# Performance work log

Hardware: AMD Instinct MI355X
Metric: run time of the kernel (lower is better)

Reference implementation:

```python
import jax, jax.numpy as jnp
import numpy as np

N_EXPERTS = 8
TOP_K = 2
C = 2048       # n_embd
H = 1024       # expert_intermediate_size
HS = 2048      # shared_expert_intermediate_size
B, T = 1, 512
SCALE = 0.02


def setup_inputs() -> dict:
    key = jax.random.key(0)
    ks = jax.random.split(key, 10)
    x = jax.random.normal(ks[0], (B, T, C), dtype=jnp.float32)
    gate_w = jax.random.normal(ks[1], (N_EXPERTS, C), dtype=jnp.float32) * SCALE
    w_gate = jax.random.normal(ks[2], (N_EXPERTS, H, C), dtype=jnp.float32) * SCALE
    w_up = jax.random.normal(ks[3], (N_EXPERTS, H, C), dtype=jnp.float32) * SCALE
    w_down = jax.random.normal(ks[4], (N_EXPERTS, C, H), dtype=jnp.float32) * SCALE
    sh_gate = jax.random.normal(ks[5], (HS, C), dtype=jnp.float32) * SCALE
    sh_up = jax.random.normal(ks[6], (HS, C), dtype=jnp.float32) * SCALE
    sh_down = jax.random.normal(ks[7], (C, HS), dtype=jnp.float32) * SCALE
    se_gate_w = jax.random.normal(ks[8], (1, C), dtype=jnp.float32) * SCALE
    return {"x": x, "gate_w": gate_w, "w_gate": w_gate, "w_up": w_up,
            "w_down": w_down, "sh_gate": sh_gate, "sh_up": sh_up,
            "sh_down": sh_down, "se_gate_w": se_gate_w}


def reference(x, gate_w, w_gate, w_up, w_down, sh_gate, sh_up, sh_down, se_gate_w):
    Bb, Tt, Cc = x.shape
    xf = x.reshape(-1, Cc)                      # (t, d)
    # routing
    scores = xf @ gate_w.T                      # (t, E)
    ew, ei = jax.lax.top_k(scores, TOP_K)       # (t, A)
    ew = jax.nn.softmax(ew, axis=-1)
    # expert FFN (dense over experts; identical math to per-token gathered einsum)
    x1 = jax.nn.silu(jnp.einsum('td,ehd->teh', xf, w_gate))
    x3 = jnp.einsum('td,ehd->teh', xf, w_up)
    expert_out = jnp.einsum('teh,edh->ted', x1 * x3, w_down)  # (t, E, d)
    # combine: routed[t] = sum_a ew[t,a] * expert_out[t, ei[t,a]]
    onehot = jax.nn.one_hot(ei, N_EXPERTS, dtype=ew.dtype)    # (t, A, E)
    comb = jnp.einsum('ta,tae->te', ew, onehot)               # (t, E)
    routed = jnp.einsum('te,ted->td', comb, expert_out)
    # shared expert (SwiGLU MLP)
    shared = (jax.nn.silu(xf @ sh_gate.T) * (xf @ sh_up.T)) @ sh_down.T
    sgate = jax.nn.sigmoid(xf @ se_gate_w.T)                  # (t, 1)
    return (routed + sgate * shared).reshape(Bb, Tt, Cc)
```

## Files before the change

kernel.cpp:

```cpp
#include <hip/hip_runtime.h>

typedef unsigned short u16;
typedef u16 u16x8 __attribute__((ext_vector_type(8)));
typedef __bf16 bf16x8 __attribute__((ext_vector_type(8)));
typedef float f32x4 __attribute__((ext_vector_type(4)));

#define NE 8

__device__ __forceinline__ unsigned pk2(float a, float b) {
  unsigned ua = __builtin_bit_cast(unsigned, a) + 0x8000u;
  unsigned ub = __builtin_bit_cast(unsigned, b) + 0x8000u;
  return __builtin_amdgcn_perm(ub, ua, 0x07060302);
}
__device__ __forceinline__ u16 f2bf(float f) {
  return (u16)((__builtin_bit_cast(unsigned, f) + 0x8000u) >> 16);
}
__device__ __forceinline__ bf16x8 ldfrag(const u16* p) {
  union { u16x8 u; bf16x8 b; } x;
  x.u = *(const u16x8*)p;
  return x.b;
}
__device__ __forceinline__ void gld16(const void* g, void* l) {
  __builtin_amdgcn_global_load_lds(
      (const __attribute__((address_space(1))) unsigned int*)g,
      (__attribute__((address_space(3))) unsigned int*)l, 16, 0, 0);
}
#define MFMA16 __builtin_amdgcn_mfma_f32_16x16x32_bf16

__global__ __launch_bounds__(64) void route_prep_kernel(
    const float* __restrict__ x, const float* __restrict__ gw,
    const float* __restrict__ segw, int* __restrict__ counts,
    int* __restrict__ ptok, float* __restrict__ pw, float* __restrict__ sgate,
    u16* __restrict__ xb) {
  int t = blockIdx.x;
  int lane = threadIdx.x;
  const float* xr = x + (size_t)t * 2048;
  u16* xbr = xb + (size_t)t * 2048;
  float s[NE];
#pragma unroll
  for (int e = 0; e < NE; e++) s[e] = 0.f;
  float sg = 0.f;
#pragma unroll
  for (int it = 0; it < 8; it++) {
    int c = it * 256 + lane * 4;
    f32x4 xv = *(const f32x4*)(xr + c);
    *(uint2*)(xbr + c) = make_uint2(pk2(xv[0], xv[1]), pk2(xv[2], xv[3]));
#pragma unroll
    for (int e = 0; e < NE; e++) {
      f32x4 wv4 = *(const f32x4*)(gw + e * 2048 + c);
      s[e] += xv[0] * wv4[0] + xv[1] * wv4[1] + xv[2] * wv4[2] + xv[3] * wv4[3];
    }
    f32x4 sv = *(const f32x4*)(segw + c);
    sg += xv[0] * sv[0] + xv[1] * sv[1] + xv[2] * sv[2] + xv[3] * sv[3];
  }
#pragma unroll
  for (int off = 32; off > 0; off >>= 1) {
#pragma unroll
    for (int e = 0; e < NE; e++) s[e] += __shfl_down(s[e], off);
    sg += __shfl_down(sg, off);
  }
  if (lane == 0) {
    int i0 = 0;
#pragma unroll
    for (int e = 1; e < NE; e++) if (s[e] > s[i0]) i0 = e;
    int i1 = (i0 == 0) ? 1 : 0;
#pragma unroll
    for (int e = 0; e < NE; e++) if (e != i0 && s[e] > s[i1]) i1 = e;
    float r = __expf(s[i1] - s[i0]);
    float w0 = 1.f / (1.f + r);
    float w1 = 1.f - w0;
    int s0 = atomicAdd(&counts[i0], 1);
    ptok[(i0 << 9) + s0] = t; pw[(i0 << 9) + s0] = w0;
    int s1 = atomicAdd(&counts[i1], 1);
    ptok[(i1 << 9) + s1] = t; pw[(i1 << 9) + s1] = w1;
    sgate[t] = 1.f / (1.f + __expf(-sg));
  }
}

__global__ __launch_bounds__(256) void gateup_kernel(
    const u16* __restrict__ xb, const float* __restrict__ Wg,
    const float* __restrict__ Wu, const float* __restrict__ SWg,
    const float* __restrict__ SWu, u16* __restrict__ hbufB,
    u16* __restrict__ hsB, const int* __restrict__ ptok,
    const int* __restrict__ counts) {
  __shared__ __align__(16) u16 As[2][128 * 64];
  __shared__ __align__(16) u16 Bs[2][32 * 64];

  int b = blockIdx.x;
  int t = threadIdx.x;
  int is_ex = (b < 2048);
  int e = 0, j, mt, cnt;
  const float *gW, *uW;
  u16* obase;
  if (is_ex) {
    e = b & 7; j = (b >> 3) & 63; mt = b >> 9;
    cnt = counts[e];
    if (mt * 128 >= cnt) return;
    gW = Wg + (size_t)(e * 1024 + j * 16) * 2048;
    uW = Wu + (size_t)(e * 1024 + j * 16) * 2048;
    obase = hbufB + (size_t)(e * 64 + j) * 8192;
  } else {
    int bs = b - 2048;
    int xcd = bs & 7; mt = (bs >> 3) & 3; j = (bs >> 5) * 8 + xcd; cnt = 512;
    gW = SWg + (size_t)(j * 16) * 2048;
    uW = SWu + (size_t)(j * 16) * 2048;
    obase = hsB + (size_t)j * 8192;
  }

  int lane = t & 63, wv = t >> 6;
  int quad = lane >> 4, l16 = lane & 15;

  const u16* aptr[4];
  int aoff[4];
#pragma unroll
  for (int i = 0; i < 4; i++) {
    int c = 4 * wv + i;
    int row = 8 * c + (lane >> 3);
    int slot = mt * 128 + row;
    int tok = is_ex ? ((slot < cnt) ? ptok[(e << 9) + slot] : 0) : slot;
    aptr[i] = xb + (size_t)tok * 2048 + (((lane & 7) ^ ((lane >> 3) & 7)) * 8);
    aoff[i] = c * 512;
  }
  const float* bsrc[2];
  int bwr[2];
#pragma unroll
  for (int i = 0; i < 2; i++) {
    int rloc = wv * 8 + i * 4 + quad;
    const float* base = (rloc < 16) ? (gW + (size_t)rloc * 2048)
                                    : (uW + (size_t)(rloc - 16) * 2048);
    bsrc[i] = base + l16 * 4;
    bwr[i] = rloc * 64 + (((l16 >> 1) ^ (rloc & 7)) * 8) + ((l16 & 1) * 4);
  }

  f32x4 accg[2] = {}, accu[2] = {};

#define GU_ISSUE(kt1, nb)                                                   \
  f32x4 bv0 = *(const f32x4*)(bsrc[0] + (kt1) * 64);                        \
  f32x4 bv1 = *(const f32x4*)(bsrc[1] + (kt1) * 64);                        \
  _Pragma("unroll") for (int i = 0; i < 4; i++)                             \
      gld16(aptr[i] + (kt1) * 64, &As[nb][aoff[i]]);                        \
  __builtin_amdgcn_sched_barrier(0);

#define GU_FINISH(nb)                                                       \
  asm volatile("s_waitcnt vmcnt(4)" ::: "memory");                          \
  *(uint2*)(&Bs[nb][bwr[0]]) =                                              \
      make_uint2(pk2(bv0[0], bv0[1]), pk2(bv0[2], bv0[3]));                 \
  *(uint2*)(&Bs[nb][bwr[1]]) =                                              \
      make_uint2(pk2(bv1[0], bv1[1]), pk2(bv1[2], bv1[3]));                 \
  asm volatile("s_waitcnt vmcnt(0) lgkmcnt(0)" ::: "memory");               \
  __builtin_amdgcn_s_barrier();                                             \
  __builtin_amdgcn_sched_barrier(0);

#define GU_COMPUTE(pb)                                                      \
  _Pragma("unroll") for (int k2 = 0; k2 < 2; k2++) {                        \
    int sl = ((k2 * 4 + quad) ^ (l16 & 7)) * 8;                             \
    bf16x8 af0 = ldfrag(&As[pb][(wv * 32 + l16) * 64 + sl]);                \
    bf16x8 af1 = ldfrag(&As[pb][(wv * 32 + 16 + l16) * 64 + sl]);           \
    bf16x8 bg = ldfrag(&Bs[pb][l16 * 64 + sl]);                             \
    bf16x8 bu = ldfrag(&Bs[pb][(16 + l16) * 64 + sl]);                      \
    accg[0] = MFMA16(af0, bg, accg[0], 0, 0, 0);                            \
    accg[1] = MFMA16(af1, bg, accg[1], 0, 0, 0);                            \
    accu[0] = MFMA16(af0, bu, accu[0], 0, 0, 0);                            \
    accu[1] = MFMA16(af1, bu, accu[1], 0, 0, 0);                            \
  }

  { GU_ISSUE(0, 0); GU_FINISH(0); }
  int pb = 0;
  for (int kt = 0; kt < 31; kt++) {
    GU_ISSUE(kt + 1, pb ^ 1);
    GU_COMPUTE(pb);
    GU_FINISH(pb ^ 1);
    pb ^= 1;
  }
  GU_COMPUTE(pb);
#undef GU_ISSUE
#undef GU_FINISH
#undef GU_COMPUTE

#pragma unroll
  for (int i = 0; i < 2; i++)
#pragma unroll
    for (int g = 0; g < 4; g++) {
      int rloc = wv * 32 + i * 16 + quad * 4 + g;
      int slot = mt * 128 + rloc;
      if (slot < cnt) {
        float gv = accg[i][g], uv = accu[i][g];
        float h = gv / (1.f + __expf(-gv)) * uv;
        obase[(size_t)slot * 16 + l16] = f2bf(h);
      }
    }
}

__global__ __launch_bounds__(256) void down_kernel(
    const u16* __restrict__ hbufB, const u16* __restrict__ hsB,
    const float* __restrict__ Wd, const float* __restrict__ SWd,
    float* __restrict__ out, const int* __restrict__ ptok,
    const float* __restrict__ pw, const int* __restrict__ counts,
    const float* __restrict__ sgate) {
  __shared__ __align__(16) u16 As[2][4 * 128 * 16];
  __shared__ __align__(16) u16 Bs[2][32 * 64];

  int b = blockIdx.x;
  int t = threadIdx.x;
  int lane = t & 63, wv = t >> 6;
  int quad = lane >> 4, l16 = lane & 15;

  if (b < 2048) {
    int e = b & 7, nt = (b >> 3) & 63, mt = b >> 9;
    int cnt = counts[e];
    if (mt * 128 >= cnt) return;
    const u16* hb = hbufB + (size_t)e * 524288;

    const u16* aptr[4];
    int aoff[4];
#pragma unroll
    for (int i = 0; i < 4; i++) {
      aptr[i] = hb + (size_t)wv * 8192 +
                (size_t)(mt * 128 + i * 32 + (lane >> 1)) * 16 +
                (((lane & 1) ^ ((lane >> 3) & 1)) * 8);
      aoff[i] = wv * 2048 + i * 512;
    }
    const float* bsrc[2];
    int bwr[2];
#pragma unroll
    for (int i = 0; i < 2; i++) {
      int rloc = wv * 8 + i * 4 + quad;
      bsrc[i] = Wd + (size_t)(e * 2048 + nt * 32 + rloc) * 1024 + l16 * 4;
      bwr[i] = rloc * 64 + (((l16 >> 1) ^ (rloc & 7)) * 8) + ((l16 & 1) * 4);
    }

    f32x4 acc[2][2] = {};

#define DE_ISSUE(kt1, nb)                                                   \
  f32x4 bv0 = *(const f32x4*)(bsrc[0] + (kt1) * 64);                        \
  f32x4 bv1 = *(const f32x4*)(bsrc[1] + (kt1) * 64);                        \
  _Pragma("unroll") for (int i = 0; i < 4; i++)                             \
      gld16(aptr[i] + (size_t)(kt1) * 32768, &As[nb][aoff[i]]);             \
  __builtin_amdgcn_sched_barrier(0);

#define DE_FINISH(nb)                                                       \
  asm volatile("s_waitcnt vmcnt(4)" ::: "memory");                          \
  *(uint2*)(&Bs[nb][bwr[0]]) =                                              \
      make_uint2(pk2(bv0[0], bv0[1]), pk2(bv0[2], bv0[3]));                 \
  *(uint2*)(&Bs[nb][bwr[1]]) =                                              \
      make_uint2(pk2(bv1[0], bv1[1]), pk2(bv1[2], bv1[3]));                 \
  asm volatile("s_waitcnt vmcnt(0) lgkmcnt(0)" ::: "memory");               \
  __builtin_amdgcn_s_barrier();                                             \
  __builtin_amdgcn_sched_barrier(0);

#define DE_COMPUTE(pb)                                                      \
  _Pragma("unroll") for (int k2 = 0; k2 < 2; k2++) {                        \
    int jsec = (k2 * 2 + (quad >> 1)) * 2048 +                              \
               (((quad & 1) ^ ((l16 >> 2) & 1)) * 8);                       \
    int sl = ((k2 * 4 + quad) ^ (l16 & 7)) * 8;                             \
    bf16x8 af0 = ldfrag(&As[pb][jsec + (wv * 32 + l16) * 16]);              \
    bf16x8 af1 = ldfrag(&As[pb][jsec + (wv * 32 + 16 + l16) * 16]);         \
    bf16x8 b0 = ldfrag(&Bs[pb][l16 * 64 + sl]);                             \
    bf16x8 b1 = ldfrag(&Bs[pb][(16 + l16) * 64 + sl]);                      \
    acc[0][0] = MFMA16(af0, b0, acc[0][0], 0, 0, 0);                        \
    acc[0][1] = MFMA16(af0, b1, acc[0][1], 0, 0, 0);                        \
    acc[1][0] = MFMA16(af1, b0, acc[1][0], 0, 0, 0);                        \
    acc[1][1] = MFMA16(af1, b1, acc[1][1], 0, 0, 0);                        \
  }

    { DE_ISSUE(0, 0); DE_FINISH(0); }
    int pb = 0;
    for (int kt = 0; kt < 15; kt++) {
      DE_ISSUE(kt + 1, pb ^ 1);
      DE_COMPUTE(pb);
      DE_FINISH(pb ^ 1);
      pb ^= 1;
    }
    DE_COMPUTE(pb);
#undef DE_ISSUE
#undef DE_FINISH
#undef DE_COMPUTE

#pragma unroll
    for (int i = 0; i < 2; i++)
#pragma unroll
      for (int jf = 0; jf < 2; jf++)
#pragma unroll
        for (int g = 0; g < 4; g++) {
          int sl = mt * 128 + wv * 32 + i * 16 + quad * 4 + g;
          if (sl < cnt) {
            int tok = ptok[(e << 9) + sl];
            int col = nt * 32 + jf * 16 + l16;
            atomicAdd(&out[(size_t)tok * 2048 + col],
                      pw[(e << 9) + sl] * acc[i][jf][g]);
          }
        }
  } else {
    int bs = b - 2048;
    int xcd = bs & 7, mt = (bs >> 3) & 3, nt = (bs >> 5) * 8 + xcd;

    const u16* aptr[4];
    int aoff[4];
#pragma unroll
    for (int i = 0; i < 4; i++) {
      aptr[i] = hsB + (size_t)wv * 8192 +
                (size_t)(mt * 128 + i * 32 + (lane >> 1)) * 16 +
                (((lane & 1) ^ ((lane >> 3) & 1)) * 8);
      aoff[i] = wv * 2048 + i * 512;
    }
    int rloc = wv * 4 + quad;
    const float* bsrc = SWd + (size_t)(nt * 16 + rloc) * 2048 + l16 * 4;
    int bwr = rloc * 64 + (((l16 >> 1) ^ (rloc & 7)) * 8) + ((l16 & 1) * 4);

    f32x4 acc[2] = {};

#define DS_ISSUE(kt1, nb)                                                   \
  f32x4 bv0 = *(const f32x4*)(bsrc + (kt1) * 64);                           \
  _Pragma("unroll") for (int i = 0; i < 4; i++)                             \
      gld16(aptr[i] + (size_t)(kt1) * 32768, &As[nb][aoff[i]]);             \
  __builtin_amdgcn_sched_barrier(0);

#define DS_FINISH(nb)                                                       \
  asm volatile("s_waitcnt vmcnt(4)" ::: "memory");                          \
  *(uint2*)(&Bs[nb][bwr]) =                                                 \
      make_uint2(pk2(bv0[0], bv0[1]), pk2(bv0[2], bv0[3]));                 \
  asm volatile("s_waitcnt vmcnt(0) lgkmcnt(0)" ::: "memory");               \
  __builtin_amdgcn_s_barrier();                                             \
  __builtin_amdgcn_sched_barrier(0);

#define DS_COMPUTE(pb)                                                      \
  _Pragma("unroll") for (int k2 = 0; k2 < 2; k2++) {                        \
    int jsec = (k2 * 2 + (quad >> 1)) * 2048 +                              \
               (((quad & 1) ^ ((l16 >> 2) & 1)) * 8);                       \
    int sl = ((k2 * 4 + quad) ^ (l16 & 7)) * 8;                             \
    bf16x8 af0 = ldfrag(&As[pb][jsec + (wv * 32 + l16) * 16]);              \
    bf16x8 af1 = ldfrag(&As[pb][jsec + (wv * 32 + 16 + l16) * 16]);         \
    bf16x8 bb = ldfrag(&Bs[pb][l16 * 64 + sl]);                             \
    acc[0] = MFMA16(af0, bb, acc[0], 0, 0, 0);                              \
    acc[1] = MFMA16(af1, bb, acc[1], 0, 0, 0);                              \
  }

    { DS_ISSUE(0, 0); DS_FINISH(0); }
    int pb = 0;
    for (int kt = 0; kt < 31; kt++) {
      DS_ISSUE(kt + 1, pb ^ 1);
      DS_COMPUTE(pb);
      DS_FINISH(pb ^ 1);
      pb ^= 1;
    }
    DS_COMPUTE(pb);
#undef DS_ISSUE
#undef DS_FINISH
#undef DS_COMPUTE

#pragma unroll
    for (int i = 0; i < 2; i++)
#pragma unroll
      for (int g = 0; g < 4; g++) {
        int row = mt * 128 + wv * 32 + i * 16 + quad * 4 + g;
        atomicAdd(&out[(size_t)row * 2048 + nt * 16 + l16],
                  sgate[row] * acc[i][g]);
      }
  }
}

extern "C" void kernel_launch(void* const* d_in, const int* in_sizes, int n_in,
                              void* d_out, int out_size, void* d_ws, size_t ws_size,
                              hipStream_t stream) {
  const float* x = (const float*)d_in[0];
  const float* gate_w = (const float*)d_in[1];
  const float* w_gate = (const float*)d_in[2];
  const float* w_up = (const float*)d_in[3];
  const float* w_down = (const float*)d_in[4];
  const float* sh_gate = (const float*)d_in[5];
  const float* sh_up = (const float*)d_in[6];
  const float* sh_down = (const float*)d_in[7];
  const float* se_gate_w = (const float*)d_in[8];
  float* out = (float*)d_out;

  char* ws = (char*)d_ws;
  int* counts = (int*)(ws + 0);
  int* ptok = (int*)(ws + 1024);
  float* pw = (float*)(ws + 1024 + 16384);
  float* sg = (float*)(ws + 1024 + 32768);
  u16* xb = (u16*)(ws + 65536);
  u16* hbufB = (u16*)(ws + 65536 + (2u << 20));
  u16* hsB = (u16*)(ws + 65536 + (10u << 20));

  hipMemsetAsync(counts, 0, 32, stream);
  hipMemsetAsync(out, 0, out_size, stream);
  route_prep_kernel<<<512, 64, 0, stream>>>(x, gate_w, se_gate_w, counts,
                                            ptok, pw, sg, xb);
  gateup_kernel<<<2560, 256, 0, stream>>>(xb, w_gate, w_up, sh_gate, sh_up,
                                          hbufB, hsB, ptok, counts);
  down_kernel<<<2560, 256, 0, stream>>>(hbufB, hsB, w_down, sh_down, out,
                                        ptok, pw, counts, sg);
}
```

Before: 347.8 us.

## Widen N tile to 64 and add triple-buffered LDS pipeline in MoE GEMMs

Both the gate/up and down kernels now compute 64-column weight tiles per block instead of 32, so each loaded activation tile is reused across twice as many columns and the grid shrinks accordingly. The double-buffered loop is replaced by a three-stage LDS ring with prefetch two k-steps ahead and a relaxed vmcnt wait, which lets weight loads overlap more compute. This raises register pressure (8 accumulators plus two staging register sets) and LDS use. It also gives fewer blocks, which may hurt occupancy and load balance across CUs.

```diff
diff --git a/kernel.cpp b/kernel.cpp
--- a/kernel.cpp
+++ b/kernel.cpp
@@ -83,28 +83,28 @@
     const float* __restrict__ SWu, u16* __restrict__ hbufB,
     u16* __restrict__ hsB, const int* __restrict__ ptok,
     const int* __restrict__ counts) {
-  __shared__ __align__(16) u16 As[2][128 * 64];
-  __shared__ __align__(16) u16 Bs[2][32 * 64];
+  __shared__ __align__(16) u16 As[3 * 8192];
+  __shared__ __align__(16) u16 Bs[3 * 4096];
 
   int b = blockIdx.x;
   int t = threadIdx.x;
-  int is_ex = (b < 2048);
+  int is_ex = (b < 1024);
   int e = 0, j, mt, cnt;
   const float *gW, *uW;
   u16* obase;
   if (is_ex) {
-    e = b & 7; j = (b >> 3) & 63; mt = b >> 9;
+    e = b & 7; j = (b >> 3) & 31; mt = b >> 8;
     cnt = counts[e];
     if (mt * 128 >= cnt) return;
-    gW = Wg + (size_t)(e * 1024 + j * 16) * 2048;
-    uW = Wu + (size_t)(e * 1024 + j * 16) * 2048;
-    obase = hbufB + (size_t)(e * 64 + j) * 8192;
+    gW = Wg + (size_t)(e * 1024 + j * 32) * 2048;
+    uW = Wu + (size_t)(e * 1024 + j * 32) * 2048;
+    obase = hbufB + (size_t)(e * 64 + 2 * j) * 8192;
   } else {
-    int bs = b - 2048;
+    int bs = b - 1024;
     int xcd = bs & 7; mt = (bs >> 3) & 3; j = (bs >> 5) * 8 + xcd; cnt = 512;
-    gW = SWg + (size_t)(j * 16) * 2048;
-    uW = SWu + (size_t)(j * 16) * 2048;
-    obase = hsB + (size_t)j * 8192;
+    gW = SWg + (size_t)(j * 32) * 2048;
+    uW = SWu + (size_t)(j * 32) * 2048;
+    obase = hsB + (size_t)(2 * j) * 8192;
   }
 
   int lane = t & 63, wv = t >> 6;
@@ -121,74 +121,114 @@
     aptr[i] = xb + (size_t)tok * 2048 + (((lane & 7) ^ ((lane >> 3) & 7)) * 8);
     aoff[i] = c * 512;
   }
-  const float* bsrc[2];
-  int bwr[2];
-#pragma unroll
-  for (int i = 0; i < 2; i++) {
-    int rloc = wv * 8 + i * 4 + quad;
-    const float* base = (rloc < 16) ? (gW + (size_t)rloc * 2048)
-                                    : (uW + (size_t)(rloc - 16) * 2048);
+  const float* bsrc[4];
+  int bwr[4];
+#pragma unroll
+  for (int i = 0; i < 4; i++) {
+    int rloc = wv * 16 + i * 4 + quad;
+    const float* base = (rloc < 32) ? (gW + (size_t)rloc * 2048)
+                                    : (uW + (size_t)(rloc - 32) * 2048);
     bsrc[i] = base + l16 * 4;
     bwr[i] = rloc * 64 + (((l16 >> 1) ^ (rloc & 7)) * 8) + ((l16 & 1) * 4);
   }
 
-  f32x4 accg[2] = {}, accu[2] = {};
-
-#define GU_ISSUE(kt1, nb)                                                   \
-  f32x4 bv0 = *(const f32x4*)(bsrc[0] + (kt1) * 64);                        \
-  f32x4 bv1 = *(const f32x4*)(bsrc[1] + (kt1) * 64);                        \
-  _Pragma("unroll") for (int i = 0; i < 4; i++)                             \
-      gld16(aptr[i] + (kt1) * 64, &As[nb][aoff[i]]);                        \
-  __builtin_amdgcn_sched_barrier(0);
-
-#define GU_FINISH(nb)                                                       \
-  asm volatile("s_waitcnt vmcnt(4)" ::: "memory");                          \
-  *(uint2*)(&Bs[nb][bwr[0]]) =                                              \
-      make_uint2(pk2(bv0[0], bv0[1]), pk2(bv0[2], bv0[3]));                 \
-  *(uint2*)(&Bs[nb][bwr[1]]) =                                              \
-      make_uint2(pk2(bv1[0], bv1[1]), pk2(bv1[2], bv1[3]));                 \
-  asm volatile("s_waitcnt vmcnt(0) lgkmcnt(0)" ::: "memory");               \
-  __builtin_amdgcn_s_barrier();                                             \
-  __builtin_amdgcn_sched_barrier(0);
-
-#define GU_COMPUTE(pb)                                                      \
+  f32x4 bA0, bA1, bA2, bA3, bB0, bB1, bB2, bB3;
+  f32x4 acc00 = {}, acc01 = {}, acc02 = {}, acc03 = {};
+  f32x4 acc10 = {}, acc11 = {}, acc12 = {}, acc13 = {};
+
+#define GU_ISSUE(kt1, ao, S)                                                \
+  S##0 = *(const f32x4*)(bsrc[0] + (kt1) * 64);                             \
+  S##1 = *(const f32x4*)(bsrc[1] + (kt1) * 64);                             \
+  S##2 = *(const f32x4*)(bsrc[2] + (kt1) * 64);                             \
+  S##3 = *(const f32x4*)(bsrc[3] + (kt1) * 64);                             \
+  gld16(aptr[0] + (kt1) * 64, &As[(ao) + aoff[0]]);                         \
+  gld16(aptr[1] + (kt1) * 64, &As[(ao) + aoff[1]]);                         \
+  gld16(aptr[2] + (kt1) * 64, &As[(ao) + aoff[2]]);                         \
+  gld16(aptr[3] + (kt1) * 64, &As[(ao) + aoff[3]]);                         \
+  __builtin_amdgcn_sched_barrier(0);
+
+#define GU_WRITEB(ao, S)                                                    \
+  *(uint2*)(&Bs[((ao) >> 1) + bwr[0]]) =                                    \
+      make_uint2(pk2(S##0[0], S##0[1]), pk2(S##0[2], S##0[3]));             \
+  *(uint2*)(&Bs[((ao) >> 1) + bwr[1]]) =                                    \
+      make_uint2(pk2(S##1[0], S##1[1]), pk2(S##1[2], S##1[3]));             \
+  *(uint2*)(&Bs[((ao) >> 1) + bwr[2]]) =                                    \
+      make_uint2(pk2(S##2[0], S##2[1]), pk2(S##2[2], S##2[3]));             \
+  *(uint2*)(&Bs[((ao) >> 1) + bwr[3]]) =                                    \
+      make_uint2(pk2(S##3[0], S##3[1]), pk2(S##3[2], S##3[3]));
+
+#define GU_COMPUTE(ao)                                                      \
   _Pragma("unroll") for (int k2 = 0; k2 < 2; k2++) {                        \
     int sl = ((k2 * 4 + quad) ^ (l16 & 7)) * 8;                             \
-    bf16x8 af0 = ldfrag(&As[pb][(wv * 32 + l16) * 64 + sl]);                \
-    bf16x8 af1 = ldfrag(&As[pb][(wv * 32 + 16 + l16) * 64 + sl]);           \
-    bf16x8 bg = ldfrag(&Bs[pb][l16 * 64 + sl]);                             \
-    bf16x8 bu = ldfrag(&Bs[pb][(16 + l16) * 64 + sl]);                      \
-    accg[0] = MFMA16(af0, bg, accg[0], 0, 0, 0);                            \
-    accg[1] = MFMA16(af1, bg, accg[1], 0, 0, 0);                            \
-    accu[0] = MFMA16(af0, bu, accu[0], 0, 0, 0);                            \
-    accu[1] = MFMA16(af1, bu, accu[1], 0, 0, 0);                            \
-  }
-
-  { GU_ISSUE(0, 0); GU_FINISH(0); }
-  int pb = 0;
-  for (int kt = 0; kt < 31; kt++) {
-    GU_ISSUE(kt + 1, pb ^ 1);
-    GU_COMPUTE(pb);
-    GU_FINISH(pb ^ 1);
-    pb ^= 1;
-  }
-  GU_COMPUTE(pb);
+    bf16x8 af0 = ldfrag(&As[(ao) + (wv * 32 + l16) * 64 + sl]);             \
+    bf16x8 af1 = ldfrag(&As[(ao) + (wv * 32 + 16 + l16) * 64 + sl]);        \
+    bf16x8 bf0 = ldfrag(&Bs[((ao) >> 1) + l16 * 64 + sl]);                  \
+    bf16x8 bf1 = ldfrag(&Bs[((ao) >> 1) + (16 + l16) * 64 + sl]);           \
+    bf16x8 bf2 = ldfrag(&Bs[((ao) >> 1) + (32 + l16) * 64 + sl]);           \
+    bf16x8 bf3 = ldfrag(&Bs[((ao) >> 1) + (48 + l16) * 64 + sl]);           \
+    acc00 = MFMA16(af0, bf0, acc00, 0, 0, 0);                               \
+    acc01 = MFMA16(af0, bf1, acc01, 0, 0, 0);                               \
+    acc02 = MFMA16(af0, bf2, acc02, 0, 0, 0);                               \
+    acc03 = MFMA16(af0, bf3, acc03, 0, 0, 0);                               \
+    acc10 = MFMA16(af1, bf0, acc10, 0, 0, 0);                               \
+    acc11 = MFMA16(af1, bf1, acc11, 0, 0, 0);                               \
+    acc12 = MFMA16(af1, bf2, acc12, 0, 0, 0);                               \
+    acc13 = MFMA16(af1, bf3, acc13, 0, 0, 0);                               \
+  }
+
+#define GU_PHASE(kt, aoC, aoI, aoW, Si, Sw)                                 \
+  GU_ISSUE((kt) + 2, aoI, Si)                                               \
+  GU_COMPUTE(aoC)                                                           \
+  asm volatile("s_waitcnt vmcnt(8)" ::: "memory");                          \
+  __builtin_amdgcn_sched_barrier(0);                                        \
+  GU_WRITEB(aoW, Sw)                                                        \
+  asm volatile("s_waitcnt lgkmcnt(0)" ::: "memory");                        \
+  __builtin_amdgcn_s_barrier();                                             \
+  __builtin_amdgcn_sched_barrier(0);
+
+  int o0 = 0, o1 = 8192, o2 = 16384;
+  GU_ISSUE(0, o0, bA)
+  GU_ISSUE(1, o1, bB)
+  asm volatile("s_waitcnt vmcnt(8)" ::: "memory");
+  __builtin_amdgcn_sched_barrier(0);
+  GU_WRITEB(o0, bA)
+  asm volatile("s_waitcnt lgkmcnt(0)" ::: "memory");
+  __builtin_amdgcn_s_barrier();
+  __builtin_amdgcn_sched_barrier(0);
+
+  for (int kt = 0; kt < 30; kt += 2) {
+    GU_PHASE(kt, o0, o2, o1, bA, bB)
+    GU_PHASE(kt + 1, o1, o0, o2, bB, bA)
+    int tmp = o0; o0 = o2; o2 = o1; o1 = tmp;
+  }
+  GU_COMPUTE(o0)
+  asm volatile("s_waitcnt vmcnt(0)" ::: "memory");
+  __builtin_amdgcn_sched_barrier(0);
+  GU_WRITEB(o1, bB)
+  asm volatile("s_waitcnt lgkmcnt(0)" ::: "memory");
+  __builtin_amdgcn_s_barrier();
+  __builtin_amdgcn_sched_barrier(0);
+  GU_COMPUTE(o1)
 #undef GU_ISSUE
-#undef GU_FINISH
+#undef GU_WRITEB
 #undef GU_COMPUTE
-
-#pragma unroll
-  for (int i = 0; i < 2; i++)
-#pragma unroll
-    for (int g = 0; g < 4; g++) {
-      int rloc = wv * 32 + i * 16 + quad * 4 + g;
-      int slot = mt * 128 + rloc;
-      if (slot < cnt) {
-        float gv = accg[i][g], uv = accu[i][g];
-        float h = gv / (1.f + __expf(-gv)) * uv;
-        obase[(size_t)slot * 16 + l16] = f2bf(h);
-      }
-    }
+#undef GU_PHASE
+
+#define GU_EPI(AG, AU, i, n)                                                \
+  _Pragma("unroll") for (int g = 0; g < 4; g++) {                           \
+    int rloc = wv * 32 + (i) * 16 + quad * 4 + g;                           \
+    int slot = mt * 128 + rloc;                                             \
+    if (slot < cnt) {                                                       \
+      float gv = AG[g], uv = AU[g];                                         \
+      float h = gv / (1.f + __expf(-gv)) * uv;                              \
+      obase[(size_t)(n) * 8192 + slot * 16 + l16] = f2bf(h);                \
+    }                                                                       \
+  }
+  GU_EPI(acc00, acc02, 0, 0)
+  GU_EPI(acc01, acc03, 0, 1)
+  GU_EPI(acc10, acc12, 1, 0)
+  GU_EPI(acc11, acc13, 1, 1)
+#undef GU_EPI
 }
 
 __global__ __launch_bounds__(256) void down_kernel(
@@ -197,16 +237,88 @@
     float* __restrict__ out, const int* __restrict__ ptok,
     const float* __restrict__ pw, const int* __restrict__ counts,
     const float* __restrict__ sgate) {
-  __shared__ __align__(16) u16 As[2][4 * 128 * 16];
-  __shared__ __align__(16) u16 Bs[2][32 * 64];
+  __shared__ __align__(16) u16 As[3 * 8192];
+  __shared__ __align__(16) u16 Bs[3 * 4096];
 
   int b = blockIdx.x;
   int t = threadIdx.x;
   int lane = t & 63, wv = t >> 6;
   int quad = lane >> 4, l16 = lane & 15;
 
-  if (b < 2048) {
-    int e = b & 7, nt = (b >> 3) & 63, mt = b >> 9;
+#define DN_ISSUE(kt1, ao, S)                                                \
+  S##0 = *(const f32x4*)(bsrc[0] + (kt1) * 64);                             \
+  S##1 = *(const f32x4*)(bsrc[1] + (kt1) * 64);                             \
+  S##2 = *(const f32x4*)(bsrc[2] + (kt1) * 64);                             \
+  S##3 = *(const f32x4*)(bsrc[3] + (kt1) * 64);                             \
+  gld16(aptr[0] + (size_t)(kt1) * 32768, &As[(ao) + aoff[0]]);              \
+  gld16(aptr[1] + (size_t)(kt1) * 32768, &As[(ao) + aoff[1]]);              \
+  gld16(aptr[2] + (size_t)(kt1) * 32768, &As[(ao) + aoff[2]]);              \
+  gld16(aptr[3] + (size_t)(kt1) * 32768, &As[(ao) + aoff[3]]);              \
+  __builtin_amdgcn_sched_barrier(0);
+
+#define DN_WRITEB(ao, S)                                                    \
+  *(uint2*)(&Bs[((ao) >> 1) + bwr[0]]) =                                    \
+      make_uint2(pk2(S##0[0], S##0[1]), pk2(S##0[2], S##0[3]));             \
+  *(uint2*)(&Bs[((ao) >> 1) + bwr[1]]) =                                    \
+      make_uint2(pk2(S##1[0], S##1[1]), pk2(S##1[2], S##1[3]));             \
+  *(uint2*)(&Bs[((ao) >> 1) + bwr[2]]) =                                    \
+      make_uint2(pk2(S##2[0], S##2[1]), pk2(S##2[2], S##2[3]));             \
+  *(uint2*)(&Bs[((ao) >> 1) + bwr[3]]) =                                    \
+      make_uint2(pk2(S##3[0], S##3[1]), pk2(S##3[2], S##3[3]));
+
+#define DN_COMPUTE(ao)                                                      \
+  _Pragma("unroll") for (int k2 = 0; k2 < 2; k2++) {                        \
+    int jsec = (k2 * 2 + (quad >> 1)) * 2048 +                              \
+               (((quad & 1) ^ ((l16 >> 2) & 1)) * 8);                       \
+    int sl = ((k2 * 4 + quad) ^ (l16 & 7)) * 8;                             \
+    bf16x8 af0 = ldfrag(&As[(ao) + jsec + (wv * 32 + l16) * 16]);           \
+    bf16x8 af1 = ldfrag(&As[(ao) + jsec + (wv * 32 + 16 + l16) * 16]);      \
+    bf16x8 bf0 = ldfrag(&Bs[((ao) >> 1) + l16 * 64 + sl]);                  \
+    bf16x8 bf1 = ldfrag(&Bs[((ao) >> 1) + (16 + l16) * 64 + sl]);           \
+    bf16x8 bf2 = ldfrag(&Bs[((ao) >> 1) + (32 + l16) * 64 + sl]);           \
+    bf16x8 bf3 = ldfrag(&Bs[((ao) >> 1) + (48 + l16) * 64 + sl]);           \
+    acc00 = MFMA16(af0, bf0, acc00, 0, 0, 0);                               \
+    acc01 = MFMA16(af0, bf1, acc01, 0, 0, 0);                               \
+    acc02 = MFMA16(af0, bf2, acc02, 0, 0, 0);                               \
+    acc03 = MFMA16(af0, bf3, acc03, 0, 0, 0);                               \
+    acc10 = MFMA16(af1, bf0, acc10, 0, 0, 0);                               \
+    acc11 = MFMA16(af1, bf1, acc11, 0, 0, 0);                               \
+    acc12 = MFMA16(af1, bf2, acc12, 0, 0, 0);                               \
+    acc13 = MFMA16(af1, bf3, acc13, 0, 0, 0);                               \
+  }
+
+#define DN_PHASE(kt, aoC, aoI, aoW, Si, Sw)                                 \
+  DN_ISSUE((kt) + 2, aoI, Si)                                               \
+  DN_COMPUTE(aoC)                                                           \
+  asm volatile("s_waitcnt vmcnt(8)" ::: "memory");                          \
+  __builtin_amdgcn_sched_barrier(0);                                        \
+  DN_WRITEB(aoW, Sw)                                                        \
+  asm volatile("s_waitcnt lgkmcnt(0)" ::: "memory");                        \
+  __builtin_amdgcn_s_barrier();                                             \
+  __builtin_amdgcn_sched_barrier(0);
+
+#define DN_PROLOGUE                                                         \
+  DN_ISSUE(0, o0, bA)                                                       \
+  DN_ISSUE(1, o1, bB)                                                       \
+  asm volatile("s_waitcnt vmcnt(8)" ::: "memory");                          \
+  __builtin_amdgcn_sched_barrier(0);                                        \
+  DN_WRITEB(o0, bA)                                                         \
+  asm volatile("s_waitcnt lgkmcnt(0)" ::: "memory");                        \
+  __builtin_amdgcn_s_barrier();                                             \
+  __builtin_amdgcn_sched_barrier(0);
+
+#define DN_TAIL                                                             \
+  DN_COMPUTE(o0)                                                            \
+  asm volatile("s_waitcnt vmcnt(0)" ::: "memory");                          \
+  __builtin_amdgcn_sched_barrier(0);                                        \
+  DN_WRITEB(o1, bB)                                                         \
+  asm volatile("s_waitcnt lgkmcnt(0)" ::: "memory");                        \
+  __builtin_amdgcn_s_barrier();                                             \
+  __builtin_amdgcn_sched_barrier(0);                                        \
+  DN_COMPUTE(o1)
+
+  if (b < 1024) {
+    int e = b & 7, nt = (b >> 3) & 31, mt = b >> 8;
     int cnt = counts[e];
     if (mt * 128 >= cnt) return;
     const u16* hb = hbufB + (size_t)e * 524288;
@@ -220,78 +332,42 @@
                 (((lane & 1) ^ ((lane >> 3) & 1)) * 8);
       aoff[i] = wv * 2048 + i * 512;
     }
-    const float* bsrc[2];
-    int bwr[2];
-#pragma unroll
-    for (int i = 0; i < 2; i++) {
-      int rloc = wv * 8 + i * 4 + quad;
-      bsrc[i] = Wd + (size_t)(e * 2048 + nt * 32 + rloc) * 1024 + l16 * 4;
+    const float* bsrc[4];
+    int bwr[4];
+#pragma unroll
+    for (int i = 0; i < 4; i++) {
+      int rloc = wv * 16 + i * 4 + quad;
+      bsrc[i] = Wd + (size_t)(e * 2048 + nt * 64 + rloc) * 1024 + l16 * 4;
       bwr[i] = rloc * 64 + (((l16 >> 1) ^ (rloc & 7)) * 8) + ((l16 & 1) * 4);
     }
 
-    f32x4 acc[2][2] = {};
-
-#define DE_ISSUE(kt1, nb)                                                   \
-  f32x4 bv0 = *(const f32x4*)(bsrc[0] + (kt1) * 64);                        \
-  f32x4 bv1 = *(const f32x4*)(bsrc[1] + (kt1) * 64);                        \
-  _Pragma("unroll") for (int i = 0; i < 4; i++)                             \
-      gld16(aptr[i] + (size_t)(kt1) * 32768, &As[nb][aoff[i]]);             \
-  __builtin_amdgcn_sched_barrier(0);
-
-#define DE_FINISH(nb)                                                       \
-  asm volatile("s_waitcnt vmcnt(4)" ::: "memory");                          \
-  *(uint2*)(&Bs[nb][bwr[0]]) =                                              \
-      make_uint2(pk2(bv0[0], bv0[1]), pk2(bv0[2], bv0[3]));                 \
-  *(uint2*)(&Bs[nb][bwr[1]]) =                                              \
-      make_uint2(pk2(bv1[0], bv1[1]), pk2(bv1[2], bv1[3]));                 \
-  asm volatile("s_waitcnt vmcnt(0) lgkmcnt(0)" ::: "memory");               \
-  __builtin_amdgcn_s_barrier();                                             \
-  __builtin_amdgcn_sched_barrier(0);
-
-#define DE_COMPUTE(pb)                                                      \
-  _Pragma("unroll") for (int k2 = 0; k2 < 2; k2++) {                        \
-    int jsec = (k2 * 2 + (quad >> 1)) * 2048 +                              \
-               (((quad & 1) ^ ((l16 >> 2) & 1)) * 8);                       \
-    int sl = ((k2 * 4 + quad) ^ (l16 & 7)) * 8;                             \
-    bf16x8 af0 = ldfrag(&As[pb][jsec + (wv * 32 + l16) * 16]);              \
-    bf16x8 af1 = ldfrag(&As[pb][jsec + (wv * 32 + 16 + l16) * 16]);         \
-    bf16x8 b0 = ldfrag(&Bs[pb][l16 * 64 + sl]);                             \
-    bf16x8 b1 = ldfrag(&Bs[pb][(16 + l16) * 64 + sl]);                      \
-    acc[0][0] = MFMA16(af0, b0, acc[0][0], 0, 0, 0);                        \
-    acc[0][1] = MFMA16(af0, b1, acc[0][1], 0, 0, 0);                        \
-    acc[1][0] = MFMA16(af1, b0, acc[1][0], 0, 0, 0);                        \
-    acc[1][1] = MFMA16(af1, b1, acc[1][1], 0, 0, 0);                        \
-  }
-
-    { DE_ISSUE(0, 0); DE_FINISH(0); }
-    int pb = 0;
-    for (int kt = 0; kt < 15; kt++) {
-      DE_ISSUE(kt + 1, pb ^ 1);
-      DE_COMPUTE(pb);
-      DE_FINISH(pb ^ 1);
-      pb ^= 1;
-    }
-    DE_COMPUTE(pb);
-#undef DE_ISSUE
-#undef DE_FINISH
-#undef DE_COMPUTE
-
-#pragma unroll
-    for (int i = 0; i < 2; i++)
-#pragma unroll
-      for (int jf = 0; jf < 2; jf++)
-#pragma unroll
-        for (int g = 0; g < 4; g++) {
-          int sl = mt * 128 + wv * 32 + i * 16 + quad * 4 + g;
-          if (sl < cnt) {
-            int tok = ptok[(e << 9) + sl];
-            int col = nt * 32 + jf * 16 + l16;
-            atomicAdd(&out[(size_t)tok * 2048 + col],
-                      pw[(e << 9) + sl] * acc[i][jf][g]);
-          }
-        }
+    f32x4 bA0, bA1, bA2, bA3, bB0, bB1, bB2, bB3;
+    f32x4 acc00 = {}, acc01 = {}, acc02 = {}, acc03 = {};
+    f32x4 acc10 = {}, acc11 = {}, acc12 = {}, acc13 = {};
+
+    int o0 = 0, o1 = 8192, o2 = 16384;
+    DN_PROLOGUE
+    for (int kt = 0; kt < 14; kt += 2) {
+      DN_PHASE(kt, o0, o2, o1, bA, bB)
+      DN_PHASE(kt + 1, o1, o0, o2, bB, bA)
+      int tmp = o0; o0 = o2; o2 = o1; o1 = tmp;
+    }
+    DN_TAIL
+
+#define DE_EPI(ACC, i, n)                                                   \
+  _Pragma("unroll") for (int g = 0; g < 4; g++) {                           \
+    int sl = mt * 128 + wv * 32 + (i) * 16 + quad * 4 + g;                  \
+    if (sl < cnt) {                                                         \
+      atomicAdd(&out[(size_t)ptok[(e << 9) + sl] * 2048 + nt * 64 +         \
+                     (n) * 16 + l16],                                       \
+                pw[(e << 9) + sl] * ACC[g]);                                \
+    }                                                                       \
+  }
+    DE_EPI(acc00, 0, 0) DE_EPI(acc01, 0, 1) DE_EPI(acc02, 0, 2) DE_EPI(acc03, 0, 3)
+    DE_EPI(acc10, 1, 0) DE_EPI(acc11, 1, 1) DE_EPI(acc12, 1, 2) DE_EPI(acc13, 1, 3)
+#undef DE_EPI
   } else {
-    int bs = b - 2048;
+    int bs = b - 1024;
     int xcd = bs & 7, mt = (bs >> 3) & 3, nt = (bs >> 5) * 8 + xcd;
 
     const u16* aptr[4];
@@ -303,60 +379,44 @@
                 (((lane & 1) ^ ((lane >> 3) & 1)) * 8);
       aoff[i] = wv * 2048 + i * 512;
     }
-    int rloc = wv * 4 + quad;
-    const float* bsrc = SWd + (size_t)(nt * 16 + rloc) * 2048 + l16 * 4;
-    int bwr = rloc * 64 + (((l16 >> 1) ^ (rloc & 7)) * 8) + ((l16 & 1) * 4);
-
-    f32x4 acc[2] = {};
-
-#define DS_ISSUE(kt1, nb)                                                   \
-  f32x4 bv0 = *(const f32x4*)(bsrc + (kt1) * 64);                           \
-  _Pragma("unroll") for (int i = 0; i < 4; i++)                             \
-      gld16(aptr[i] + (size_t)(kt1) * 32768, &As[nb][aoff[i]]);             \
-  __builtin_amdgcn_sched_barrier(0);
-
-#define DS_FINISH(nb)                                                       \
-  asm volatile("s_waitcnt vmcnt(4)" ::: "memory");                          \
-  *(uint2*)(&Bs[nb][bwr]) =                                                 \
-      make_uint2(pk2(bv0[0], bv0[1]), pk2(bv0[2], bv0[3]));                 \
-  asm volatile("s_waitcnt vmcnt(0) lgkmcnt(0)" ::: "memory");               \
-  __builtin_amdgcn_s_barrier();                                             \
-  __builtin_amdgcn_sched_barrier(0);
-
-#define DS_COMPUTE(pb)                                                      \
-  _Pragma("unroll") for (int k2 = 0; k2 < 2; k2++) {                        \
-    int jsec = (k2 * 2 + (quad >> 1)) * 2048 +                              \
-               (((quad & 1) ^ ((l16 >> 2) & 1)) * 8);                       \
-    int sl = ((k2 * 4 + quad) ^ (l16 & 7)) * 8;                             \
-    bf16x8 af0 = ldfrag(&As[pb][jsec + (wv * 32 + l16) * 16]);              \
-    bf16x8 af1 = ldfrag(&As[pb][jsec + (wv * 32 + 16 + l16) * 16]);         \
-    bf16x8 bb = ldfrag(&Bs[pb][l16 * 64 + sl]);                             \
-    acc[0] = MFMA16(af0, bb, acc[0], 0, 0, 0);                              \
-    acc[1] = MFMA16(af1, bb, acc[1], 0, 0, 0);                              \
-  }
-
-    { DS_ISSUE(0, 0); DS_FINISH(0); }
-    int pb = 0;
-    for (int kt = 0; kt < 31; kt++) {
-      DS_ISSUE(kt + 1, pb ^ 1);
-      DS_COMPUTE(pb);
-      DS_FINISH(pb ^ 1);
-      pb ^= 1;
-    }
-    DS_COMPUTE(pb);
-#undef DS_ISSUE
-#undef DS_FINISH
-#undef DS_COMPUTE
-
-#pragma unroll
-    for (int i = 0; i < 2; i++)
-#pragma unroll
-      for (int g = 0; g < 4; g++) {
-        int row = mt * 128 + wv * 32 + i * 16 + quad * 4 + g;
-        atomicAdd(&out[(size_t)row * 2048 + nt * 16 + l16],
-                  sgate[row] * acc[i][g]);
-      }
-  }
+    const float* bsrc[4];
+    int bwr[4];
+#pragma unroll
+    for (int i = 0; i < 4; i++) {
+      int rloc = wv * 16 + i * 4 + quad;
+      bsrc[i] = SWd + (size_t)(nt * 64 + rloc) * 2048 + l16 * 4;
+      bwr[i] = rloc * 64 + (((l16 >> 1) ^ (rloc & 7)) * 8) + ((l16 & 1) * 4);
+    }
+
+    f32x4 bA0, bA1, bA2, bA3, bB0, bB1, bB2, bB3;
+    f32x4 acc00 = {}, acc01 = {}, acc02 = {}, acc03 = {};
+    f32x4 acc10 = {}, acc11 = {}, acc12 = {}, acc13 = {};
+
+    int o0 = 0, o1 = 8192, o2 = 16384;
+    DN_PROLOGUE
+    for (int kt = 0; kt < 30; kt += 2) {
+      DN_PHASE(kt, o0, o2, o1, bA, bB)
+      DN_PHASE(kt + 1, o1, o0, o2, bB, bA)
+      int tmp = o0; o0 = o2; o2 = o1; o1 = tmp;
+    }
+    DN_TAIL
+
+#define DS_EPI(ACC, i, n)                                                   \
+  _Pragma("unroll") for (int g = 0; g < 4; g++) {                           \
+    int row = mt * 128 + wv * 32 + (i) * 16 + quad * 4 + g;                 \
+    atomicAdd(&out[(size_t)row * 2048 + nt * 64 + (n) * 16 + l16],          \
+              sgate[row] * ACC[g]);                                         \
+  }
+    DS_EPI(acc00, 0, 0) DS_EPI(acc01, 0, 1) DS_EPI(acc02, 0, 2) DS_EPI(acc03, 0, 3)
+    DS_EPI(acc10, 1, 0) DS_EPI(acc11, 1, 1) DS_EPI(acc12, 1, 2) DS_EPI(acc13, 1, 3)
+#undef DS_EPI
+  }
+#undef DN_ISSUE
+#undef DN_WRITEB
+#undef DN_COMPUTE
+#undef DN_PHASE
+#undef DN_PROLOGUE
+#undef DN_TAIL
 }
 
 extern "C" void kernel_launch(void* const* d_in, const int* in_sizes, int n_in,
@@ -386,8 +446,8 @@
   hipMemsetAsync(out, 0, out_size, stream);
   route_prep_kernel<<<512, 64, 0, stream>>>(x, gate_w, se_gate_w, counts,
                                             ptok, pw, sg, xb);
-  gateup_kernel<<<2560, 256, 0, stream>>>(xb, w_gate, w_up, sh_gate, sh_up,
+  gateup_kernel<<<1280, 256, 0, stream>>>(xb, w_gate, w_up, sh_gate, sh_up,
                                           hbufB, hsB, ptok, counts);
-  down_kernel<<<2560, 256, 0, stream>>>(hbufB, hsB, w_down, sh_down, out,
+  down_kernel<<<1152, 256, 0, stream>>>(hbufB, hsB, w_down, sh_down, out,
                                         ptok, pw, counts, sg);
 }
```

Result: no change. 353.8 us (+1.7%).
